# Optimization experiments

Hardware: AMD Instinct MI355X
Metric: run time of the kernel (lower is better)

Reference implementation:

```python
import jax, jax.numpy as jnp
import numpy as np

B, N, IN, HD, NH, L, OUT = 256, 128, 9, 128, 8, 4, 60
DH = HD // NH
ALPHA = 0.6
EPS = 1e-5

def _ln(x, g, b):
    m = jnp.mean(x, axis=-1, keepdims=True)
    v = jnp.mean((x - m) ** 2, axis=-1, keepdims=True)
    return (x - m) * jax.lax.rsqrt(v + EPS) * g + b

def setup_inputs():
    key = jax.random.key(0)
    ks = jax.random.split(key, 30)
    p = lambda i, s: jax.random.normal(ks[i], s, jnp.float32) * 0.02
    strong = (jax.random.uniform(ks[25], (N, N)) < 0.15).astype(jnp.float32)
    strong = jnp.maximum(strong, jnp.eye(N, dtype=jnp.float32))  # self loops
    weak_mask = (jax.random.uniform(ks[26], (N, N)) < 0.10).astype(jnp.float32)
    return {
        'x': jax.random.normal(ks[0], (B, N, IN), jnp.float32),
        'conv_w': p(1, (HD, IN)), 'conv_b': p(2, (HD,)),
        'bn_gamma': jnp.ones((HD,), jnp.float32), 'bn_beta': jnp.zeros((HD,), jnp.float32),
        'bn_mean': jnp.zeros((HD,), jnp.float32), 'bn_var': jnp.ones((HD,), jnp.float32),
        'W': p(3, (L, HD, HD)), 'a_src': p(4, (L, NH, DH)), 'a_dst': p(5, (L, NH, DH)),
        'ln_g': jnp.ones((L, HD), jnp.float32), 'ln_b': jnp.zeros((L, HD), jnp.float32),
        'ffn_w1': p(6, (L, HD, 2 * HD)), 'ffn_b1': p(7, (L, 2 * HD)),
        'ffn_w2': p(8, (L, 2 * HD, HD)), 'ffn_b2': p(9, (L, HD)),
        'norm_g': jnp.ones((HD,), jnp.float32), 'norm_b': jnp.zeros((HD,), jnp.float32),
        'proj_w': p(10, (HD, HD)), 'proj_b': p(11, (HD,)),
        'head_w1': p(12, (HD, HD // 2)), 'head_b1': p(13, (HD // 2,)),
        'head_w2': p(14, (HD // 2, OUT)), 'head_b2': p(15, (OUT,)),
        'strong_adj': strong, 'weak_mask': weak_mask,
        'weak_param': p(16, (N, N)), 'edge_weight_adj': p(17, (N, N)),
    }

def reference(x, conv_w, conv_b, bn_gamma, bn_beta, bn_mean, bn_var, W, a_src, a_dst, ln_g, ln_b, ffn_w1, ffn_b1, ffn_w2, ffn_b2, norm_g, norm_b, proj_w, proj_b, head_w1, head_b1, head_w2, head_b2, strong_adj, weak_mask, weak_param, edge_weight_adj):
    # embedding: Conv1d(k=1) == per-node linear, then eval-mode BatchNorm1d + ReLU
    h = jnp.einsum('bni,oi->bno', x, conv_w) + conv_b  # [B,N,HD]
    h = (h - bn_mean) * jax.lax.rsqrt(bn_var + EPS) * bn_gamma + bn_beta
    h = jax.nn.relu(h)
    # weak adjacency: learnable gated edges, row-normalized (shared across layers)
    Aw = jax.nn.sigmoid(weak_param) * weak_mask
    Aw = Aw / (jnp.sum(Aw, axis=-1, keepdims=True) + EPS)  # [N,N]
    for i in range(L):
        res = h
        hp = jnp.einsum('bnd,de->bne', h, W[i]).reshape(B, N, NH, DH)
        s = jnp.einsum('bnhd,hd->bnh', hp, a_src[i])
        t = jnp.einsum('bnhd,hd->bnh', hp, a_dst[i])
        e = jax.nn.leaky_relu(s[:, :, None, :] + t[:, None, :, :], 0.2)  # [B,N,N,H]
        e = e + edge_weight_adj[None, :, :, None]  # learned per-edge bias
        e = jnp.where(strong_adj[None, :, :, None] > 0, e, jnp.float32(-1e9))
        att = jax.nn.softmax(e, axis=2)  # softmax over neighbors j
        strong_out = jnp.einsum('bijh,bjhd->bihd', att, hp)
        weak_out = jnp.einsum('ij,bjhd->bihd', Aw, hp)
        g = jax.nn.relu(ALPHA * strong_out + (1.0 - ALPHA) * weak_out).reshape(B, N, HD)
        g = _ln(g, ln_g[i], ln_b[i])
        g = jax.nn.relu(g @ ffn_w1[i] + ffn_b1[i]) @ ffn_w2[i] + ffn_b2[i]
        h = g + res
    h = _ln(h, norm_g, norm_b)
    h = h @ proj_w + proj_b
    h = jnp.mean(h, axis=1)  # mean-pool over nodes -> [B,HD]
    h = jax.nn.relu(h @ head_w1 + head_b1)
    return h @ head_w2 + head_b2  # [B,OUT]
```

## Files before the change

kernel.cpp:

```cpp
#include <hip/hip_runtime.h>
#include <hip/hip_bf16.h>

typedef __hip_bfloat16 bf16;
typedef unsigned short u16;
typedef __attribute__((ext_vector_type(8))) short bfrag;
typedef __attribute__((ext_vector_type(4))) float cfrag;

union BF { bfrag v; u16 u[8]; unsigned w[4]; };
union CF { cfrag v; float f[4]; };

#define MFMA(a,b,c) __builtin_amdgcn_mfma_f32_16x16x32_bf16(a,b,c,0,0,0)

#define BB   256
#define NN   128
#define IND  9
#define HDD  128
#define LLY  4
#define OUTD 60
#define LOG2E 1.44269504f
#define STR  136

__device__ __forceinline__ float b2f(bf16 v){ return __bfloat162float(v); }
__device__ __forceinline__ float u2f(u16 u){ return __uint_as_float(((unsigned)u) << 16); }
__device__ __forceinline__ u16 f2bf_bits(float f){
    unsigned u = __float_as_uint(f);
    return (u16)((u + 0x7FFFu + ((u >> 16) & 1u)) >> 16);
}
__device__ __forceinline__ unsigned pk2(float a, float b){
    union { __hip_bfloat162 h; unsigned u; } c;
    c.h = __float22bfloat162_rn(make_float2(a, b));
    return c.u;
}
__device__ __forceinline__ float wave_sum(float v){
    #pragma unroll
    for (int m = 32; m; m >>= 1) v += __shfl_xor(v, m, 64);
    return v;
}
__device__ __forceinline__ float ldin(const void* p, int i, bool isbf){
    return isbf ? b2f(((const bf16*)p)[i]) : ((const float*)p)[i];
}

struct SrcPtrs { const void* p[28]; };

__device__ const int NCV_OFF[19] = {0,1152,1280,1408,1536,1664,1792,2304,2816,3840,
                                    4352,4480,4608,20992,21120,29312,29376,33216,33276};
__device__ const int NCV_SRC[18] = {1,2,3,4,5,6,10,11,13,15,16,17,18,19,20,21,22,23};

__global__ __launch_bounds__(256) void k_prep(
    SrcPtrs S, float* __restrict__ pf,
    u16* __restrict__ WT, u16* __restrict__ w1T, u16* __restrict__ w2T,
    u16* __restrict__ WAb, u16* __restrict__ ew2, u16* __restrict__ Aw16,
    int* __restrict__ flagOut)
{
    __shared__ float tile[64][65];
    const unsigned* xw = (const unsigned*)S.p[0];
    int lane = threadIdx.x & 63;
    int cnt = 0;
    for (int i = lane; i < 512; i += 64) {
        float v = __uint_as_float((xw[i] & 0xFFFFu) << 16);
        if (!(fabsf(v) < 32.f)) cnt++;
    }
    bool isbf = wave_sum((float)cnt) < 16.f;
    if (blockIdx.x == 0 && threadIdx.x == 0) *flagOut = isbf ? 1 : 0;

    int blk = blockIdx.x, tid = threadIdx.x;
    if (blk < 131) {
        int idx = blk * 256 + tid;
        if (idx < 33276) {
            int y = 17;
            #pragma unroll 1
            for (int t = 1; t < 18; t++) if (idx < NCV_OFF[t]) { y = t - 1; break; }
            pf[idx] = ldin(S.p[NCV_SRC[y]], idx - NCV_OFF[y], isbf);
        }
    } else if (blk < 211) {
        const void* src; u16* dst; int K, N, k0, n0;
        if (blk < 147) {
            int t = blk - 131, l = t >> 2, tt = t & 3;
            src = (const char*)S.p[7] + (size_t)l * 16384 * (isbf ? 2 : 4);
            dst = WT + l * 16384; K = 128; N = 128; k0 = (tt >> 1) * 64; n0 = (tt & 1) * 64;
        } else if (blk < 179) {
            int t = blk - 147, l = t >> 3, tt = t & 7;
            src = (const char*)S.p[12] + (size_t)l * 32768 * (isbf ? 2 : 4);
            dst = w1T + l * 32768; K = 128; N = 256; k0 = (tt >> 2) * 64; n0 = (tt & 3) * 64;
        } else {
            int t = blk - 179, l = t >> 3, tt = t & 7;
            src = (const char*)S.p[14] + (size_t)l * 32768 * (isbf ? 2 : 4);
            dst = w2T + l * 32768; K = 256; N = 128; k0 = (tt & 3) * 64; n0 = (tt >> 2) * 64;
        }
        int ty = tid >> 6, tx = tid & 63;
        #pragma unroll 4
        for (int i = 0; i < 16; i++) {
            int row = ty * 16 + i;
            tile[row][tx] = ldin(src, (k0 + row) * N + n0 + tx, isbf);
        }
        __syncthreads();
        #pragma unroll 4
        for (int i = 0; i < 16; i++) {
            int row = ty * 16 + i;
            dst[(n0 + row) * K + k0 + tx] = f2bf_bits(tile[tx][row]);
        }
    } else if (blk < 243) {
        int j = (blk - 211) * 256 + tid;
        int l = j >> 11, r = j & 2047, n = r >> 7, k = r & 127;
        int h = n & 7;
        const void* ap = (n < 8) ? S.p[8] : S.p[9];
        float sacc = 0.f;
        #pragma unroll 1
        for (int d = 0; d < 16; d++)
            sacc += ldin(S.p[7], l * 16384 + k * 128 + h * 16 + d, isbf)
                  * ldin(ap, l * 128 + h * 16 + d, isbf);
        WAb[j] = f2bf_bits(sacc);
    } else if (blk < 307) {
        int j = (blk - 243) * 256 + tid;
        float sav = ldin(S.p[24], j, isbf);
        float ewv = ldin(S.p[27], j, isbf);
        ew2[j] = f2bf_bits(sav > 0.f ? ewv * LOG2E : -1e30f);
    } else {
        __shared__ float red[2];
        int i = blk - 307, j = tid & 127;
        float v = 0.f;
        if (tid < 128) {
            float wmv = ldin(S.p[25], i * 128 + j, isbf);
            float wpv = ldin(S.p[26], i * 128 + j, isbf);
            v = wmv / (1.f + __expf(-wpv));
            float sm = wave_sum(v);
            if ((tid & 63) == 0) red[tid >> 6] = sm;
        }
        __syncthreads();
        if (tid < 128) {
            float tot = red[0] + red[1];
            Aw16[i * 128 + j] = f2bf_bits(0.4f * v / (tot + 1e-5f));
        }
    }
}

#define LDSB (128*STR*2*2 + 128*132*4 + 2560*4)
__global__ __launch_bounds__(512, 1) void k_net(
    const void* __restrict__ xraw, const int* __restrict__ flag,
    const float* __restrict__ pf,
    const u16* __restrict__ WTg, const u16* __restrict__ WAbg,
    const u16* __restrict__ Awg, const u16* __restrict__ ew2g,
    const u16* __restrict__ w1Tg, const u16* __restrict__ w2Tg,
    void* __restrict__ outv)
{
    extern __shared__ __align__(16) char smem[];
    u16* U1 = (u16*)smem;
    u16* U2 = U1 + 128 * STR;
    float* hres = (float*)(U2 + 128 * STR);
    float* st2  = hres + 128 * 132;
    float* s2   = st2;
    u16*   t2u  = (u16*)(st2 + 1024);

    const int b = blockIdx.x;
    const int tid = threadIdx.x, lane = tid & 63, wv = tid >> 6;
    const int l15 = lane & 15, kg = lane >> 4;
    const int wrow = wv * 16;
    const int arow = wrow + l15;
    const bool isbf = (*flag != 0);

    {
        float xr[4][IND];
        #pragma unroll
        for (int r = 0; r < 4; r++) {
            int bn = b * NN + wrow + kg * 4 + r;
            #pragma unroll
            for (int k = 0; k < IND; k++) xr[r][k] = ldin(xraw, bn * IND + k, isbf);
        }
        #pragma unroll 1
        for (int nt = 0; nt < 8; nt++) {
            int d = nt * 16 + l15;
            float cwreg[IND];
            #pragma unroll
            for (int k = 0; k < IND; k++) cwreg[k] = pf[d * IND + k];
            float scale = rsqrtf(pf[1664 + d] + 1e-5f) * pf[1280 + d];
            float bias  = pf[1408 + d] - pf[1536 + d] * scale;
            float cbd   = pf[1152 + d];
            #pragma unroll
            for (int r = 0; r < 4; r++) {
                float a = cbd;
                #pragma unroll
                for (int k = 0; k < IND; k++) a = fmaf(xr[r][k], cwreg[k], a);
                a = fmaxf(fmaf(a, scale, bias), 0.f);
                int row = wrow + kg * 4 + r;
                hres[row * 132 + d] = a;
                U1[row * STR + d] = f2bf_bits(a);
            }
        }
    }

    #pragma unroll 1
    for (int l = 0; l < LLY; l++) {
        const u16* WT  = WTg  + l * 16384;
        const u16* WAb = WAbg + l * 2048;
        const u16* w1T = w1Tg + l * 32768;
        const u16* w2T = w2Tg + l * 32768;
        const float* fb1 = pf + 2816 + l * 256;
        const float* fb2 = pf + 3840 + l * 128;
        const float* lng = pf + 1792 + l * 128;
        const float* lnb = pf + 2304 + l * 128;

        __syncthreads();

        {
            CF acc[8], ast;
            #pragma unroll
            for (int r = 0; r < 4; r++) ast.f[r] = 0.f;
            #pragma unroll
            for (int nt = 0; nt < 8; nt++)
                #pragma unroll
                for (int r = 0; r < 4; r++) acc[nt].f[r] = 0.f;
            #pragma unroll
            for (int kk = 0; kk < 4; kk++) {
                bfrag af  = *(const bfrag*)&U1[arow * STR + kk*32 + kg*8];
                bfrag wab = *(const bfrag*)&WAb[l15 * 128 + kk*32 + kg*8];
                ast.v = MFMA(af, wab, ast.v);
                #pragma unroll
                for (int nt = 0; nt < 8; nt++) {
                    bfrag bw = *(const bfrag*)&WT[(nt*16 + l15) * 128 + kk*32 + kg*8];
                    acc[nt].v = MFMA(af, bw, acc[nt].v);
                }
            }
            #pragma unroll
            for (int nt = 0; nt < 8; nt++) {
                int col = nt*16 + l15;
                #pragma unroll
                for (int rp = 0; rp < 2; rp++) {
                    int row = wrow + kg*4 + rp*2;
                    *(unsigned*)&U2[col * STR + row] = pk2(acc[nt].f[rp*2], acc[nt].f[rp*2+1]);
                }
            }
            #pragma unroll
            for (int r = 0; r < 4; r++) {
                int node = wrow + kg*4 + r;
                float v = ast.f[r] * LOG2E;
                if (l15 < 8) s2[l15 * 128 + node] = v;
                else         t2u[(l15 - 8) * 128 + node] = f2bf_bits(v);
            }
        }
        __syncthreads();

        CF accS[8];
        #pragma unroll
        for (int nt = 0; nt < 8; nt++)
            #pragma unroll
            for (int r = 0; r < 4; r++) accS[nt].f[r] = 0.f;
        #pragma unroll
        for (int kk = 0; kk < 4; kk++) {
            bfrag awf = *(const bfrag*)&Awg[arow * 128 + kk*32 + kg*8];
            #pragma unroll
            for (int nt = 0; nt < 8; nt++) {
                bfrag hb2 = *(const bfrag*)&U2[(nt*16 + l15) * STR + kk*32 + kg*8];
                accS[nt].v = MFMA(awf, hb2, accS[nt].v);
            }
        }

        BF e2f[4];
        #pragma unroll
        for (int kk = 0; kk < 4; kk++)
            e2f[kk].v = *(const bfrag*)&ew2g[arow * 128 + kk*32 + kg*8];
        #pragma unroll
        for (int h = 0; h < 8; h++) {
            bfrag hb[4];
            #pragma unroll
            for (int kk = 0; kk < 4; kk++)
                hb[kk] = *(const bfrag*)&U2[(h*16 + l15) * STR + kk*32 + kg*8];
            float sA = s2[h * 128 + arow];
            float pv[4][8];
            float sm = 0.f;
            #pragma unroll
            for (int kk = 0; kk < 4; kk++) {
                BF tb; tb.v = *(const bfrag*)&t2u[h * 128 + kk*32 + kg*8];
                #pragma unroll
                for (int j = 0; j < 8; j++) {
                    float x2 = sA + u2f(tb.u[j]);
                    float lk = fmaxf(x2, 0.2f * x2);
                    float p = __builtin_amdgcn_exp2f(lk + u2f(e2f[kk].u[j]));
                    pv[kk][j] = p; sm += p;
                }
            }
            sm += __shfl_xor(sm, 16, 64);
            sm += __shfl_xor(sm, 32, 64);
            float sc = 0.6f * __builtin_amdgcn_rcpf(sm);
            #pragma unroll
            for (int kk = 0; kk < 4; kk++) {
                BF pb;
                #pragma unroll
                for (int q = 0; q < 4; q++)
                    pb.w[q] = pk2(pv[kk][2*q] * sc, pv[kk][2*q+1] * sc);
                accS[h].v = MFMA(pb.v, hb[kk], accS[h].v);
            }
        }

        #pragma unroll
        for (int r = 0; r < 4; r++) {
            float s1 = 0.f, sq = 0.f;
            #pragma unroll
            for (int nt = 0; nt < 8; nt++) {
                float x = fmaxf(accS[nt].f[r], 0.f);
                accS[nt].f[r] = x; s1 += x; sq = fmaf(x, x, sq);
            }
            #pragma unroll
            for (int m = 1; m <= 8; m <<= 1) { s1 += __shfl_xor(s1, m, 64); sq += __shfl_xor(sq, m, 64); }
            float mu = s1 * (1.f / 128.f);
            float var = sq * (1.f / 128.f) - mu * mu;
            float rs = rsqrtf(fmaxf(var, 0.f) + 1e-5f);
            #pragma unroll
            for (int nt = 0; nt < 8; nt++) {
                int col = nt*16 + l15;
                U1[(wrow + kg*4 + r) * STR + col] =
                    f2bf_bits(fmaf((accS[nt].f[r] - mu) * rs, lng[col], lnb[col]));
            }
        }

        __syncthreads();

        CF acc2[8];
        #pragma unroll
        for (int nt = 0; nt < 8; nt++)
            #pragma unroll
            for (int r = 0; r < 4; r++) acc2[nt].f[r] = 0.f;
        #pragma unroll
        for (int nh = 0; nh < 2; nh++) {
            CF a1[8];
            #pragma unroll
            for (int nt = 0; nt < 8; nt++)
                #pragma unroll
                for (int r = 0; r < 4; r++) a1[nt].f[r] = 0.f;
            #pragma unroll
            for (int kk = 0; kk < 4; kk++) {
                bfrag gf = *(const bfrag*)&U1[arow * STR + kk*32 + kg*8];
                #pragma unroll
                for (int nt = 0; nt < 8; nt++) {
                    bfrag wf = *(const bfrag*)&w1T[(nh*128 + nt*16 + l15) * 128 + kk*32 + kg*8];
                    a1[nt].v = MFMA(gf, wf, a1[nt].v);
                }
            }
            #pragma unroll
            for (int nt = 0; nt < 8; nt++) {
                int col = nt*16 + l15;
                float b1v = fb1[nh*128 + col];
                #pragma unroll
                for (int r = 0; r < 4; r++)
                    U2[(wrow + kg*4 + r) * STR + col] = f2bf_bits(fmaxf(a1[nt].f[r] + b1v, 0.f));
            }
            #pragma unroll
            for (int kk = 0; kk < 4; kk++) {
                bfrag hf = *(const bfrag*)&U2[arow * STR + kk*32 + kg*8];
                #pragma unroll
                for (int nt = 0; nt < 8; nt++) {
                    bfrag wf = *(const bfrag*)&w2T[(nt*16 + l15) * 256 + nh*128 + kk*32 + kg*8];
                    acc2[nt].v = MFMA(hf, wf, acc2[nt].v);
                }
            }
        }

        #pragma unroll
        for (int nt = 0; nt < 8; nt++) {
            int col = nt*16 + l15;
            float b2v = fb2[col];
            #pragma unroll
            for (int r = 0; r < 4; r++) {
                int row = wrow + kg*4 + r;
                float hv = hres[row * 132 + col] + acc2[nt].f[r] + b2v;
                hres[row * 132 + col] = hv;
                if (l < LLY - 1) U1[row * STR + col] = f2bf_bits(hv);
            }
        }
    }

    const float* ng = pf + 4352;
    const float* nb = pf + 4480;
    float pacc[8];
    #pragma unroll
    for (int nt = 0; nt < 8; nt++) pacc[nt] = 0.f;
    #pragma unroll
    for (int r = 0; r < 4; r++) {
        int row = wrow + kg*4 + r;
        float hvv[8];
        float s1 = 0.f, sq = 0.f;
        #pragma unroll
        for (int nt = 0; nt < 8; nt++) {
            float x = hres[row * 132 + nt*16 + l15];
            hvv[nt] = x; s1 += x; sq = fmaf(x, x, sq);
        }
        #pragma unroll
        for (int m = 1; m <= 8; m <<= 1) { s1 += __shfl_xor(s1, m, 64); sq += __shfl_xor(sq, m, 64); }
        float mu = s1 * (1.f / 128.f);
        float var = sq * (1.f / 128.f) - mu * mu;
        float rs = rsqrtf(fmaxf(var, 0.f) + 1e-5f);
        #pragma unroll
        for (int nt = 0; nt < 8; nt++)
            pacc[nt] += fmaf((hvv[nt] - mu) * rs, ng[nt*16 + l15], nb[nt*16 + l15]);
    }
    #pragma unroll
    for (int nt = 0; nt < 8; nt++) {
        pacc[nt] += __shfl_xor(pacc[nt], 16, 64);
        pacc[nt] += __shfl_xor(pacc[nt], 32, 64);
    }
    __syncthreads();
    if (kg == 0) {
        #pragma unroll
        for (int nt = 0; nt < 8; nt++) st2[wv * 128 + nt*16 + l15] = pacc[nt];
    }
    __syncthreads();
    if (tid < 128) {
        float tot = 0.f;
        #pragma unroll
        for (int w = 0; w < 8; w++) tot += st2[w * 128 + tid];
        st2[1024 + tid] = tot * (1.f / 128.f);
    }
    __syncthreads();
    {
        int e = tid & 127, kq = tid >> 7;
        float a = 0.f;
        #pragma unroll 4
        for (int k = kq * 32; k < kq * 32 + 32; k++)
            a = fmaf(st2[1024 + k], pf[4608 + k * 128 + e], a);
        st2[1152 + kq * 128 + e] = a;
    }
    __syncthreads();
    if (tid < 128)
        st2[1664 + tid] = st2[1152 + tid] + st2[1280 + tid] + st2[1408 + tid] + st2[1536 + tid]
                        + pf[20992 + tid];
    __syncthreads();
    if (tid < 64) {
        float a1 = pf[29312 + tid];
        #pragma unroll 4
        for (int k = 0; k < 128; k++) a1 = fmaf(st2[1664 + k], pf[21120 + k * 64 + tid], a1);
        st2[1792 + tid] = fmaxf(a1, 0.f);
    }
    __syncthreads();
    if (tid < OUTD) {
        float a2 = pf[33216 + tid];
        #pragma unroll 4
        for (int k = 0; k < 64; k++) a2 = fmaf(st2[1792 + k], pf[29376 + k * OUTD + tid], a2);
        if (isbf) ((bf16*)outv)[b * OUTD + tid] = __float2bfloat16(a2);
        else      ((float*)outv)[b * OUTD + tid] = a2;
    }
}

extern "C" void kernel_launch(void* const* d_in, const int* in_sizes, int n_in,
                              void* d_out, int out_size, void* d_ws, size_t ws_size,
                              hipStream_t stream)
{
    float* ws = (float*)d_ws;
    float* pf = ws;
    int*   flag = (int*)(ws + 33280);
    u16* WT16   = (u16*)(ws + 33536);
    u16* w1T16  = WT16 + 65536;
    u16* w2T16  = w1T16 + 131072;
    u16* WAb16  = w2T16 + 131072;
    u16* Aw16   = WAb16 + 8192;
    u16* ew2p   = Aw16 + 16384;

    SrcPtrs S;
    for (int i = 0; i < 28; i++) S.p[i] = d_in[i];

    hipFuncSetAttribute((const void*)k_net,
                        hipFuncAttributeMaxDynamicSharedMemorySize, LDSB);

    k_prep<<<435, 256, 0, stream>>>(S, pf, WT16, w1T16, w2T16, WAb16, ew2p, Aw16, flag);
    k_net<<<BB, 512, LDSB, stream>>>(d_in[0], flag, pf,
                                     WT16, WAb16, Aw16, ew2p, w1T16, w2T16, d_out);
}
```

Before: 353.3 us.

## Stream attention MFMAs per k-chunk with deferred softmax normalization; split FFN1 accumulators

Attention probabilities are now packed to bf16 and fed to the MFMA as soon as each 32-column chunk is computed. The per-row 0.6/sum scale is written to shared memory and applied to the accumulators afterwards, instead of buffering all 32 probabilities per lane. The weak-adjacency GEMM moves after that scaling so it is not rescaled, and the FFN first GEMM runs in two groups of four accumulators. The aim is to cut register pressure (launch bounds 512,1) and avoid spills. In exchange, probabilities are unnormalized when rounded to bf16, which slightly changes precision, and each wave does an extra shared-memory round trip for the scales.

```diff
diff --git a/kernel.cpp b/kernel.cpp
--- a/kernel.cpp
+++ b/kernel.cpp
@@ -150,6 +150,7 @@
     float* st2  = hres + 128 * 132;
     float* s2   = st2;
     u16*   t2u  = (u16*)(st2 + 1024);
+    float* invb = st2 + 1536;
 
     const int b = blockIdx.x;
     const int tid = threadIdx.x, lane = tid & 63, wv = tid >> 6;
@@ -244,50 +245,49 @@
         for (int nt = 0; nt < 8; nt++)
             #pragma unroll
             for (int r = 0; r < 4; r++) accS[nt].f[r] = 0.f;
-        #pragma unroll
-        for (int kk = 0; kk < 4; kk++) {
-            bfrag awf = *(const bfrag*)&Awg[arow * 128 + kk*32 + kg*8];
-            #pragma unroll
-            for (int nt = 0; nt < 8; nt++) {
-                bfrag hb2 = *(const bfrag*)&U2[(nt*16 + l15) * STR + kk*32 + kg*8];
-                accS[nt].v = MFMA(awf, hb2, accS[nt].v);
-            }
-        }
-
         BF e2f[4];
         #pragma unroll
         for (int kk = 0; kk < 4; kk++)
             e2f[kk].v = *(const bfrag*)&ew2g[arow * 128 + kk*32 + kg*8];
         #pragma unroll
         for (int h = 0; h < 8; h++) {
-            bfrag hb[4];
-            #pragma unroll
-            for (int kk = 0; kk < 4; kk++)
-                hb[kk] = *(const bfrag*)&U2[(h*16 + l15) * STR + kk*32 + kg*8];
             float sA = s2[h * 128 + arow];
-            float pv[4][8];
             float sm = 0.f;
             #pragma unroll
             for (int kk = 0; kk < 4; kk++) {
+                bfrag hb = *(const bfrag*)&U2[(h*16 + l15) * STR + kk*32 + kg*8];
                 BF tb; tb.v = *(const bfrag*)&t2u[h * 128 + kk*32 + kg*8];
+                BF pb;
+                float p0[8];
                 #pragma unroll
                 for (int j = 0; j < 8; j++) {
                     float x2 = sA + u2f(tb.u[j]);
                     float lk = fmaxf(x2, 0.2f * x2);
                     float p = __builtin_amdgcn_exp2f(lk + u2f(e2f[kk].u[j]));
-                    pv[kk][j] = p; sm += p;
-                }
+                    p0[j] = p; sm += p;
+                }
+                #pragma unroll
+                for (int q = 0; q < 4; q++) pb.w[q] = pk2(p0[2*q], p0[2*q+1]);
+                accS[h].v = MFMA(pb.v, hb, accS[h].v);
             }
             sm += __shfl_xor(sm, 16, 64);
             sm += __shfl_xor(sm, 32, 64);
-            float sc = 0.6f * __builtin_amdgcn_rcpf(sm);
-            #pragma unroll
-            for (int kk = 0; kk < 4; kk++) {
-                BF pb;
-                #pragma unroll
-                for (int q = 0; q < 4; q++)
-                    pb.w[q] = pk2(pv[kk][2*q] * sc, pv[kk][2*q+1] * sc);
-                accS[h].v = MFMA(pb.v, hb[kk], accS[h].v);
+            invb[h * 128 + arow] = 0.6f * __builtin_amdgcn_rcpf(sm);
+        }
+        #pragma unroll
+        for (int h = 0; h < 8; h++) {
+            const float4 iv = *(const float4*)&invb[h * 128 + wrow + kg*4];
+            accS[h].f[0] *= iv.x; accS[h].f[1] *= iv.y;
+            accS[h].f[2] *= iv.z; accS[h].f[3] *= iv.w;
+        }
+
+        #pragma unroll
+        for (int kk = 0; kk < 4; kk++) {
+            bfrag awf = *(const bfrag*)&Awg[arow * 128 + kk*32 + kg*8];
+            #pragma unroll
+            for (int nt = 0; nt < 8; nt++) {
+                bfrag hb2 = *(const bfrag*)&U2[(nt*16 + l15) * STR + kk*32 + kg*8];
+                accS[nt].v = MFMA(awf, hb2, accS[nt].v);
             }
         }
 
@@ -321,27 +321,32 @@
             for (int r = 0; r < 4; r++) acc2[nt].f[r] = 0.f;
         #pragma unroll
         for (int nh = 0; nh < 2; nh++) {
-            CF a1[8];
-            #pragma unroll
-            for (int nt = 0; nt < 8; nt++)
-                #pragma unroll
-                for (int r = 0; r < 4; r++) a1[nt].f[r] = 0.f;
-            #pragma unroll
-            for (int kk = 0; kk < 4; kk++) {
-                bfrag gf = *(const bfrag*)&U1[arow * STR + kk*32 + kg*8];
-                #pragma unroll
-                for (int nt = 0; nt < 8; nt++) {
-                    bfrag wf = *(const bfrag*)&w1T[(nh*128 + nt*16 + l15) * 128 + kk*32 + kg*8];
-                    a1[nt].v = MFMA(gf, wf, a1[nt].v);
-                }
-            }
-            #pragma unroll
-            for (int nt = 0; nt < 8; nt++) {
-                int col = nt*16 + l15;
-                float b1v = fb1[nh*128 + col];
-                #pragma unroll
-                for (int r = 0; r < 4; r++)
-                    U2[(wrow + kg*4 + r) * STR + col] = f2bf_bits(fmaxf(a1[nt].f[r] + b1v, 0.f));
+            #pragma unroll
+            for (int g4 = 0; g4 < 2; g4++) {
+                CF a1[4];
+                #pragma unroll
+                for (int q = 0; q < 4; q++)
+                    #pragma unroll
+                    for (int r = 0; r < 4; r++) a1[q].f[r] = 0.f;
+                #pragma unroll
+                for (int kk = 0; kk < 4; kk++) {
+                    bfrag gf = *(const bfrag*)&U1[arow * STR + kk*32 + kg*8];
+                    #pragma unroll
+                    for (int q = 0; q < 4; q++) {
+                        int n = nh*128 + (g4*4+q)*16 + l15;
+                        bfrag wf = *(const bfrag*)&w1T[n * 128 + kk*32 + kg*8];
+                        a1[q].v = MFMA(gf, wf, a1[q].v);
+                    }
+                }
+                #pragma unroll
+                for (int q = 0; q < 4; q++) {
+                    int col = (g4*4+q)*16 + l15;
+                    float b1v = fb1[nh*128 + col];
+                    #pragma unroll
+                    for (int r = 0; r < 4; r++)
+                        U2[(wrow + kg*4 + r) * STR + col] =
+                            f2bf_bits(fmaxf(a1[q].f[r] + b1v, 0.f));
+                }
             }
             #pragma unroll
             for (int kk = 0; kk < 4; kk++) {
```

Result: slower. 382.4 us (+8.2%).
